# Optimization experiments

Hardware: AMD Instinct MI355X
Metric: run time of the kernel (lower is better)

## Reference

```python
import jax, jax.numpy as jnp
import numpy as np

N, A, H, W = 8, 3, 336, 336
IMG_W, IMG_H = 1333.0, 800.0
PRE_TOP_K = 2000
POST_NMS_TOP_N = 1000
NMS_THR = 0.7
MIN_SIZE = 0.0
TO_REMOVE = 1.0
XFORM_CLIP = float(np.log(1000.0 / 16.0))
NEG = -1e9


def setup_inputs() -> dict:
    key = jax.random.key(0)
    k1, k2, k3, k4, k5, k6 = jax.random.split(key, 6)
    M = A * H * W
    x1 = jax.random.uniform(k1, (N, M)) * (IMG_W - 1.0)
    y1 = jax.random.uniform(k2, (N, M)) * (IMG_H - 1.0)
    bw = jax.random.uniform(k3, (N, M)) * 256.0 + 4.0
    bh = jax.random.uniform(k4, (N, M)) * 256.0 + 4.0
    anchors = jnp.stack([x1, y1, x1 + bw, y1 + bh], axis=-1).astype(jnp.float32)
    logits = jax.random.normal(k5, (N, A, H, W), dtype=jnp.float32)
    bbox_reg = jax.random.normal(k6, (N, A * 4, H, W), dtype=jnp.float32) * 0.25
    return {"anchors": anchors, "logits": logits, "bbox_reg": bbox_reg}


def _decode(anchors, deltas):
    # anchors, deltas: [..., 4] in xyxy / (dx,dy,dw,dh)
    w = anchors[..., 2] - anchors[..., 0] + TO_REMOVE
    h = anchors[..., 3] - anchors[..., 1] + TO_REMOVE
    cx = anchors[..., 0] + 0.5 * w
    cy = anchors[..., 1] + 0.5 * h
    dx, dy, dw, dh = deltas[..., 0], deltas[..., 1], deltas[..., 2], deltas[..., 3]
    dw = jnp.minimum(dw, XFORM_CLIP)
    dh = jnp.minimum(dh, XFORM_CLIP)
    pcx = dx * w + cx
    pcy = dy * h + cy
    pw = jnp.exp(dw) * w
    ph = jnp.exp(dh) * h
    return jnp.stack([pcx - 0.5 * pw, pcy - 0.5 * ph,
                      pcx + 0.5 * pw - 1.0, pcy + 0.5 * ph - 1.0], axis=-1)


def _nms_single(boxes, scores):
    # boxes: [K,4], scores: [K] (invalid entries already set to NEG)
    areas = (boxes[:, 2] - boxes[:, 0] + TO_REMOVE) * (boxes[:, 3] - boxes[:, 1] + TO_REMOVE)

    def step(live, _):
        j = jnp.argmax(live)
        sj = live[j]
        bj = boxes[j]
        xx1 = jnp.maximum(bj[0], boxes[:, 0])
        yy1 = jnp.maximum(bj[1], boxes[:, 1])
        xx2 = jnp.minimum(bj[2], boxes[:, 2])
        yy2 = jnp.minimum(bj[3], boxes[:, 3])
        inter = jnp.maximum(xx2 - xx1 + TO_REMOVE, 0.0) * jnp.maximum(yy2 - yy1 + TO_REMOVE, 0.0)
        iou = inter / (areas[j] + areas - inter)
        live = jnp.where(iou > NMS_THR, NEG, live)
        live = live.at[j].set(NEG)
        valid = sj > NEG * 0.5
        return live, (jnp.where(valid, bj, 0.0), jnp.where(valid, sj, 0.0))

    _, (sel_boxes, sel_scores) = jax.lax.scan(step, scores, None, length=POST_NMS_TOP_N)
    return sel_boxes, sel_scores


def _forward(anchors, logits, bbox_reg):
    n, a, h, w = logits.shape
    # objectness scores: [N, A*H*W], ordered as (H, W, A) like the torch permute
    scores = jax.nn.sigmoid(jnp.transpose(logits, (0, 2, 3, 1)).reshape(n, -1))
    reg = bbox_reg.reshape(n, a, 4, h, w)
    reg = jnp.transpose(reg, (0, 3, 4, 1, 2)).reshape(n, -1, 4)
    k = min(scores.shape[1], PRE_TOP_K)
    top_scores, idx = jax.lax.top_k(scores, k)  # sorted descending
    reg_k = jnp.take_along_axis(reg, idx[..., None], axis=1)
    anc_k = jnp.take_along_axis(anchors, idx[..., None], axis=1)
    props = _decode(anc_k, reg_k)
    x1 = jnp.clip(props[..., 0], 0.0, IMG_W - 1.0)
    y1 = jnp.clip(props[..., 1], 0.0, IMG_H - 1.0)
    x2 = jnp.clip(props[..., 2], 0.0, IMG_W - 1.0)
    y2 = jnp.clip(props[..., 3], 0.0, IMG_H - 1.0)
    clipped = jnp.stack([x1, y1, x2, y2], axis=-1)
    ws = x2 - x1 + TO_REMOVE
    hs = y2 - y1 + TO_REMOVE
    keep = (ws >= MIN_SIZE) & (hs >= MIN_SIZE)
    sc = jnp.where(keep, top_scores, NEG)
    sel_boxes, sel_scores = jax.vmap(_nms_single)(clipped, sc)
    # [N, POST_NMS_TOP_N, 5] = boxes + score
    return jnp.concatenate([sel_boxes, sel_scores[..., None]], axis=-1)


def reference(anchors, logits, bbox_reg):
    return _forward(anchors, logits, bbox_reg)
```

## Files before the change

### kernel.cpp

```cpp
#include <hip/hip_runtime.h>
#include <stdint.h>

#define N_BATCH 8
#define A_ 3
#define H_ 336
#define W_ 336
#define HW_ (H_*W_)
#define M_ (A_*HW_)
#define K_TOP 2000
#define POST_N 1000
#define NMS_THR_ 0.7f
#define NEG_ (-1e9f)
#define VALID_THR_ (-5e8f)
#define CAND_CAP 4096
#define NBINS 4096
#define BIN_SHIFT 20
#define HBLK 32
#define SEG_ (M_/HBLK)
#define XCLIP 4.135166556742356f

#define NPAD 2048
#define NW 32
#define NCHUNK 32
#define RING 4
#define RBLK 128

typedef unsigned long long u64;

__device__ __forceinline__ unsigned int flip_key(float x) {
    unsigned int u = __float_as_uint(x);
    return (u & 0x80000000u) ? ~u : (u | 0x80000000u);
}
__device__ __forceinline__ float unflip_key(unsigned int k) {
    unsigned int u = (k & 0x80000000u) ? (k & 0x7fffffffu) : ~k;
    return __uint_as_float(u);
}

__device__ __forceinline__ void gload_lds16(const u64* g, u64* l) {
    __builtin_amdgcn_global_load_lds(
        (const __attribute__((address_space(1))) unsigned int*)(const void*)g,
        (__attribute__((address_space(3))) unsigned int*)(void*)l,
        16, 0, 0);
}

__global__ __launch_bounds__(512) void k_hist(const float* __restrict__ logits,
                                              unsigned short* __restrict__ ghist,
                                              unsigned int* __restrict__ cnt) {
    __shared__ unsigned int h[NBINS];
    int n = blockIdx.y, b = blockIdx.x;
    if (b == 0 && threadIdx.x == 0) cnt[n] = 0;
    for (int i = threadIdx.x; i < NBINS; i += 512) h[i] = 0;
    __syncthreads();
    const float4* lp = (const float4*)(logits + (size_t)n * M_ + (size_t)b * SEG_);
    const int nq = SEG_ / 4;
    for (int q = threadIdx.x; q < nq; q += 512) {
        float4 v = lp[q];
        atomicAdd(&h[flip_key(v.x) >> BIN_SHIFT], 1u);
        atomicAdd(&h[flip_key(v.y) >> BIN_SHIFT], 1u);
        atomicAdd(&h[flip_key(v.z) >> BIN_SHIFT], 1u);
        atomicAdd(&h[flip_key(v.w) >> BIN_SHIFT], 1u);
    }
    __syncthreads();
    unsigned short* gp = ghist + ((size_t)n * HBLK + b) * NBINS;
    for (int i = threadIdx.x; i < NBINS; i += 512) gp[i] = (unsigned short)h[i];
}

__global__ __launch_bounds__(512) void k_compact(const float* __restrict__ logits,
                                                 const unsigned short* __restrict__ ghist,
                                                 unsigned int* __restrict__ cnt,
                                                 u64* __restrict__ cand) {
    __shared__ unsigned int binsum[NBINS];
    __shared__ unsigned int part[512];
    __shared__ unsigned int scanb[512];
    __shared__ u64 buf[CAND_CAP];
    __shared__ unsigned int lcnt;
    __shared__ unsigned int gbase;
    __shared__ int Bsh;
    int n = blockIdx.y, b = blockIdx.x;
    int t = threadIdx.x;
    if (t == 0) lcnt = 0;
    const unsigned short* base = ghist + (size_t)n * HBLK * NBINS;
    for (int i = t; i < NBINS; i += 512) {
        unsigned int s = 0;
        #pragma unroll 8
        for (int sb = 0; sb < HBLK; ++sb) s += base[(size_t)sb * NBINS + i];
        binsum[i] = s;
    }
    __syncthreads();
    int hi = NBINS - 8 * t;
    int lo = hi - 8;
    unsigned int s = 0;
    for (int bb = lo; bb < hi; ++bb) s += binsum[bb];
    part[t] = s;
    scanb[t] = s;
    __syncthreads();
    for (int off = 1; off < 512; off <<= 1) {
        unsigned int v = scanb[t];
        unsigned int addv = (t >= off) ? scanb[t - off] : 0u;
        __syncthreads();
        scanb[t] = v + addv;
        __syncthreads();
    }
    unsigned int incl = scanb[t];
    unsigned int prefix = incl - part[t];
    if (prefix < K_TOP && incl >= K_TOP) {
        unsigned int acc = prefix;
        for (int bb = hi - 1; bb >= lo; --bb) {
            unsigned int c = binsum[bb];
            if (acc + c >= K_TOP) { Bsh = bb; break; }
            acc += c;
        }
    }
    __syncthreads();
    unsigned int B = (unsigned int)Bsh;
    const int qbase = b * SEG_;
    const float4* lp = (const float4*)(logits + (size_t)n * M_ + (size_t)qbase);
    const int nq = SEG_ / 4;
    for (int q = t; q < nq; q += 512) {
        float4 v = lp[q];
        float vv[4] = {v.x, v.y, v.z, v.w};
        #pragma unroll
        for (int e = 0; e < 4; ++e) {
            unsigned int u = flip_key(vv[e]);
            if ((u >> BIN_SHIFT) >= B) {
                int qq = qbase + q * 4 + e;
                int a = qq / HW_;
                int hw = qq - a * HW_;
                unsigned int m = (unsigned int)(hw * A_ + a);
                unsigned int pos = atomicAdd(&lcnt, 1u);
                if (pos < CAND_CAP)
                    buf[pos] = ((u64)u << 32) | (unsigned int)(~m);
            }
        }
    }
    __syncthreads();
    unsigned int L = (lcnt < CAND_CAP) ? lcnt : CAND_CAP;
    if (t == 0) gbase = atomicAdd(&cnt[n], L);
    __syncthreads();
    u64* cp = cand + (size_t)n * CAND_CAP;
    for (unsigned int i = t; i < L; i += 512) {
        unsigned int pos = gbase + i;
        if (pos < CAND_CAP) cp[pos] = buf[i];
    }
}

__global__ __launch_bounds__(512) void k_rank(const u64* __restrict__ cand,
                                              const unsigned int* __restrict__ cnt,
                                              const float* __restrict__ anchors,
                                              const float* __restrict__ breg,
                                              float4* __restrict__ boxes,
                                              float* __restrict__ scores,
                                              float* __restrict__ areas) {
    __shared__ u64 keys[CAND_CAP];
    __shared__ unsigned short psum[512];
    int n = blockIdx.y;
    int bx = blockIdx.x;
    unsigned int Cu = cnt[n];
    int C = (Cu < CAND_CAP) ? (int)Cu : CAND_CAP;
    if (bx * RBLK >= C) return;
    const u64* cp = cand + (size_t)n * CAND_CAP;
    for (int i = threadIdx.x; i < C; i += 512) keys[i] = cp[i];
    __syncthreads();
    int t = threadIdx.x;
    int tq = t & 3;
    int cl = t >> 2;
    int ci = bx * RBLK + cl;
    unsigned int r = 0;
    u64 ki = 0;
    if (ci < C) {
        ki = keys[ci];
        int j = tq;
        for (; j + 12 < C; j += 16) {
            r += (keys[j] > ki);
            r += (keys[j + 4] > ki);
            r += (keys[j + 8] > ki);
            r += (keys[j + 12] > ki);
        }
        for (; j < C; j += 4) r += (keys[j] > ki);
    }
    psum[t] = (unsigned short)r;
    __syncthreads();
    if (tq == 0 && ci < C) {
        unsigned int rank = (unsigned int)psum[t] + psum[t + 1] + psum[t + 2] + psum[t + 3];
        if (rank < K_TOP) {
            unsigned int u = (unsigned int)(ki >> 32);
            unsigned int m = ~((unsigned int)ki);
            float logit = unflip_key(u);
            int a = (int)(m % 3u);
            int hw = (int)(m / 3u);
            float4 anc = ((const float4*)anchors)[(size_t)n * M_ + m];
            size_t rb = ((size_t)n * 12 + a * 4) * HW_ + hw;
            float dx = breg[rb];
            float dy = breg[rb + (size_t)HW_];
            float dw = breg[rb + (size_t)2 * HW_];
            float dh = breg[rb + (size_t)3 * HW_];
            float score = 1.0f / (1.0f + expf(-logit));
            float w = anc.z - anc.x + 1.0f;
            float h = anc.w - anc.y + 1.0f;
            float cx = anc.x + 0.5f * w;
            float cy = anc.y + 0.5f * h;
            dw = fminf(dw, XCLIP);
            dh = fminf(dh, XCLIP);
            float pcx = dx * w + cx;
            float pcy = dy * h + cy;
            float pw = expf(dw) * w;
            float ph = expf(dh) * h;
            float x1 = pcx - 0.5f * pw;
            float y1 = pcy - 0.5f * ph;
            float x2 = pcx + 0.5f * pw - 1.0f;
            float y2 = pcy + 0.5f * ph - 1.0f;
            x1 = fminf(fmaxf(x1, 0.0f), 1332.0f);
            y1 = fminf(fmaxf(y1, 0.0f), 799.0f);
            x2 = fminf(fmaxf(x2, 0.0f), 1332.0f);
            y2 = fminf(fmaxf(y2, 0.0f), 799.0f);
            float ww = x2 - x1 + 1.0f;
            float hh = y2 - y1 + 1.0f;
            bool keep = (ww >= 0.0f) && (hh >= 0.0f);
            int g = n * K_TOP + (int)rank;
            boxes[g] = make_float4(x1, y1, x2, y2);
            scores[g] = keep ? score : NEG_;
            areas[g] = ww * hh;
        }
    }
}

#define JT 512
#define RT 64
__global__ __launch_bounds__(256) void k_edges(const float4* __restrict__ boxes,
                                               const float* __restrict__ areas,
                                               u64* __restrict__ adj) {
    int n = blockIdx.z;
    int by = blockIdx.y;
    int bx = blockIdx.x;
    if (by > bx * 8 + 7) return;
    __shared__ float4 jb[JT];
    __shared__ float ja[JT];
    int r0 = by * RT;
    int j0 = bx * JT;
    for (int j = threadIdx.x; j < JT; j += 256) {
        int jj = j0 + j;
        if (jj < K_TOP) {
            jb[j] = boxes[(size_t)n * K_TOP + jj];
            ja[j] = areas[(size_t)n * K_TOP + jj];
        } else {
            jb[j] = make_float4(-1e8f, -1e8f, -1e8f, -1e8f);
            ja[j] = 0.0f;
        }
    }
    __syncthreads();
    int i = r0 + (threadIdx.x >> 2);
    if (i >= K_TOP) return;
    float4 bi = boxes[(size_t)n * K_TOP + i];
    float ai = areas[(size_t)n * K_TOP + i];
    #pragma unroll
    for (int rep = 0; rep < 2; ++rep) {
        int wl = (threadIdx.x & 3) + rep * 4;
        u64 bits = 0;
        int base = wl * 64;
        #pragma unroll 8
        for (int b = 0; b < 64; ++b) {
            float4 bj = jb[base + b];
            float xx1 = fmaxf(bi.x, bj.x);
            float yy1 = fmaxf(bi.y, bj.y);
            float xx2 = fminf(bi.z, bj.z);
            float yy2 = fminf(bi.w, bj.w);
            float inter = fmaxf(xx2 - xx1 + 1.0f, 0.0f) * fmaxf(yy2 - yy1 + 1.0f, 0.0f);
            float iou = inter / (ai + ja[base + b] - inter);
            bits |= ((u64)(iou > NMS_THR_)) << b;
        }
        adj[((size_t)n * NPAD + i) * NW + (j0 >> 6) + wl] = bits;
    }
}

__global__ __launch_bounds__(256) void k_resolve(const float4* __restrict__ boxes,
                                                 const float* __restrict__ scores,
                                                 const u64* __restrict__ adj,
                                                 float* __restrict__ out) {
    __shared__ u64 ring[RING][64 * NW];
    __shared__ float sls[NPAD];
    __shared__ unsigned char alive[NPAD];
    __shared__ int ready[RING];
    __shared__ int progress;
    __shared__ unsigned int scanbuf[256];
    int n = blockIdx.x;
    int tid = threadIdx.x;
    int wave = tid >> 6, lane = tid & 63;
    const u64* ab = adj + (size_t)n * NPAD * NW;

    for (int i = tid; i < NPAD; i += 256) {
        sls[i] = (i < K_TOP) ? scores[(size_t)n * K_TOP + i] : NEG_;
        alive[i] = 0;
    }
    if (tid < RING) ready[tid] = 0;
    if (tid == 0) progress = 0;
    __syncthreads();

    if (wave == 0) {
        u64 supreg = 0;
        int survTot = 0;
        for (int c = 0; c < NCHUNK; ++c) {
            int slot = c & (RING - 1);
            while (__hip_atomic_load(&ready[slot], __ATOMIC_ACQUIRE,
                                     __HIP_MEMORY_SCOPE_WORKGROUP) != c + 1)
                __builtin_amdgcn_s_sleep(1);
            int k = lane;
            int gi = c * 64 + k;
            u64 colk = ring[slot][k * NW + c];
            u64 supc = __shfl(supreg, c, 64);
            bool validk = (sls[gi] > VALID_THR_) && !((supc >> k) & 1ull);
            u64 below = (k == 0) ? 0ull : ((1ull << k) - 1ull);
            u64 rel = colk & below;
            bool a = validk;
            u64 am = __ballot(a);
            while (true) {
                bool anew = validk && ((am & rel) == 0ull);
                u64 am2 = __ballot(anew);
                if (am2 == am) { a = anew; break; }
                am = am2;
            }
            alive[gi] = a ? 1 : 0;
            int nal = (int)__popcll(am);
            survTot += nal;
            if (survTot >= POST_N) {
                if (lane == 0)
                    __hip_atomic_store(&progress, NCHUNK, __ATOMIC_RELEASE,
                                       __HIP_MEMORY_SCOPE_WORKGROUP);
                break;
            }
            int w = lane & 31, half = lane >> 5;
            u64 acc = 0;
            u64 m = am & (half ? 0xAAAAAAAAAAAAAAAAull : 0x5555555555555555ull);
            while (m) {
                int k1 = __ffsll((unsigned long long)m) - 1; m &= m - 1;
                int k2 = k1, k3 = k1, k4 = k1;
                if (m) { k2 = __ffsll((unsigned long long)m) - 1; m &= m - 1; }
                if (m) { k3 = __ffsll((unsigned long long)m) - 1; m &= m - 1; }
                if (m) { k4 = __ffsll((unsigned long long)m) - 1; m &= m - 1; }
                u64 r1 = ring[slot][k1 * NW + w];
                u64 r2 = ring[slot][k2 * NW + w];
                u64 r3 = ring[slot][k3 * NW + w];
                u64 r4 = ring[slot][k4 * NW + w];
                acc |= r1 | r2 | r3 | r4;
            }
            acc |= __shfl_down(acc, 32);
            if (lane < 32) supreg |= acc;
            if (lane == 0)
                __hip_atomic_store(&progress, c + 1, __ATOMIC_RELEASE,
                                   __HIP_MEMORY_SCOPE_WORKGROUP);
        }
    } else {
        for (int c = wave - 1; c < NCHUNK; c += 3) {
            int slot = c & (RING - 1);
            int p;
            while ((p = __hip_atomic_load(&progress, __ATOMIC_ACQUIRE,
                                          __HIP_MEMORY_SCOPE_WORKGROUP)) < c - 3)
                __builtin_amdgcn_s_sleep(1);
            if (p >= NCHUNK) break;
            const u64* src = ab + (size_t)c * 64 * NW + lane * 2;
            u64* dst = &ring[slot][0];
            #pragma unroll
            for (int it = 0; it < 16; ++it)
                gload_lds16(src + (size_t)it * 128, dst + it * 128);
            __builtin_amdgcn_s_waitcnt(0);
            if (lane == 0)
                __hip_atomic_store(&ready[slot], c + 1, __ATOMIC_RELEASE,
                                   __HIP_MEMORY_SCOPE_WORKGROUP);
        }
    }
    __syncthreads();

    int i0 = tid * 8;
    unsigned int c2 = 0;
    for (int i = i0; i < i0 + 8; ++i) c2 += alive[i];
    scanbuf[tid] = c2;
    __syncthreads();
    for (int off = 1; off < 256; off <<= 1) {
        unsigned int v = scanbuf[tid];
        unsigned int addv = (tid >= off) ? scanbuf[tid - off] : 0u;
        __syncthreads();
        scanbuf[tid] = v + addv;
        __syncthreads();
    }
    unsigned int r = scanbuf[tid] - c2;
    unsigned int total = scanbuf[255];
    float* op = out + (size_t)n * POST_N * 5;
    const float4* bb = boxes + (size_t)n * K_TOP;
    for (int i = i0; i < i0 + 8; ++i) {
        if (alive[i]) {
            if (r < POST_N) {
                float4 b = bb[i];
                op[r * 5 + 0] = b.x;
                op[r * 5 + 1] = b.y;
                op[r * 5 + 2] = b.z;
                op[r * 5 + 3] = b.w;
                op[r * 5 + 4] = sls[i];
            }
            r++;
        }
    }
    unsigned int S = (total > POST_N) ? POST_N : total;
    for (unsigned int q = S + tid; q < POST_N; q += 256) {
        op[q * 5 + 0] = 0.0f;
        op[q * 5 + 1] = 0.0f;
        op[q * 5 + 2] = 0.0f;
        op[q * 5 + 3] = 0.0f;
        op[q * 5 + 4] = 0.0f;
    }
}

extern "C" void kernel_launch(void* const* d_in, const int* in_sizes, int n_in,
                              void* d_out, int out_size, void* d_ws, size_t ws_size,
                              hipStream_t stream) {
    const float* anchors = (const float*)d_in[0];
    const float* logits  = (const float*)d_in[1];
    const float* breg    = (const float*)d_in[2];
    float* out = (float*)d_out;
    char* ws = (char*)d_ws;

    unsigned int* cnt     = (unsigned int*)(ws);
    unsigned short* ghist = (unsigned short*)(ws + 128);
    u64* cand             = (u64*)(ws + 2097280);
    u64* adj              = (u64*)(ws + 128);
    float4* boxes         = (float4*)(ws + 4194432);
    float* scores         = (float*)(ws + 4450432);
    float* areas          = (float*)(ws + 4514432);

    k_hist<<<dim3(HBLK, 8), 512, 0, stream>>>(logits, ghist, cnt);
    k_compact<<<dim3(HBLK, 8), 512, 0, stream>>>(logits, ghist, cnt, cand);
    k_rank<<<dim3(CAND_CAP / RBLK, 8), 512, 0, stream>>>(cand, cnt, anchors, breg,
                                                         boxes, scores, areas);
    k_edges<<<dim3(NPAD / JT, NPAD / RT, 8), 256, 0, stream>>>(boxes, areas, adj);
    k_resolve<<<8, 256, 0, stream>>>(boxes, scores, adj, out);
}
```

Before: 197.7 us.

## Split candidates into above-threshold and boundary-bin sets; dual LDS histograms; unroll suppression gather

After: 195.7 us. Within noise of the previous version (-1.1%).

```diff
diff --git a/kernel.cpp b/kernel.cpp
--- a/kernel.cpp
+++ b/kernel.cpp
@@ -46,23 +46,26 @@
 __global__ __launch_bounds__(512) void k_hist(const float* __restrict__ logits,
                                               unsigned short* __restrict__ ghist,
                                               unsigned int* __restrict__ cnt) {
-    __shared__ unsigned int h[NBINS];
+    __shared__ unsigned int h[2][NBINS];
     int n = blockIdx.y, b = blockIdx.x;
-    if (b == 0 && threadIdx.x == 0) cnt[n] = 0;
-    for (int i = threadIdx.x; i < NBINS; i += 512) h[i] = 0;
-    __syncthreads();
+    if (b == 0 && threadIdx.x < 2) cnt[n * 2 + threadIdx.x] = 0;
+    unsigned int* hf = &h[0][0];
+    for (int i = threadIdx.x; i < 2 * NBINS; i += 512) hf[i] = 0;
+    __syncthreads();
+    int wp = (threadIdx.x >> 6) & 1;
     const float4* lp = (const float4*)(logits + (size_t)n * M_ + (size_t)b * SEG_);
     const int nq = SEG_ / 4;
     for (int q = threadIdx.x; q < nq; q += 512) {
         float4 v = lp[q];
-        atomicAdd(&h[flip_key(v.x) >> BIN_SHIFT], 1u);
-        atomicAdd(&h[flip_key(v.y) >> BIN_SHIFT], 1u);
-        atomicAdd(&h[flip_key(v.z) >> BIN_SHIFT], 1u);
-        atomicAdd(&h[flip_key(v.w) >> BIN_SHIFT], 1u);
+        atomicAdd(&h[wp][flip_key(v.x) >> BIN_SHIFT], 1u);
+        atomicAdd(&h[wp][flip_key(v.y) >> BIN_SHIFT], 1u);
+        atomicAdd(&h[wp][flip_key(v.z) >> BIN_SHIFT], 1u);
+        atomicAdd(&h[wp][flip_key(v.w) >> BIN_SHIFT], 1u);
     }
     __syncthreads();
     unsigned short* gp = ghist + ((size_t)n * HBLK + b) * NBINS;
-    for (int i = threadIdx.x; i < NBINS; i += 512) gp[i] = (unsigned short)h[i];
+    for (int i = threadIdx.x; i < NBINS; i += 512)
+        gp[i] = (unsigned short)(h[0][i] + h[1][i]);
 }
 
 __global__ __launch_bounds__(512) void k_compact(const float* __restrict__ logits,
@@ -72,13 +75,13 @@
     __shared__ unsigned int binsum[NBINS];
     __shared__ unsigned int part[512];
     __shared__ unsigned int scanb[512];
-    __shared__ u64 buf[CAND_CAP];
-    __shared__ unsigned int lcnt;
-    __shared__ unsigned int gbase;
+    __shared__ u64 bufHi[2048];
+    __shared__ u64 bufLo[4096];
+    __shared__ unsigned int lcntHi, lcntLo, gbaseHi, gbaseLo;
     __shared__ int Bsh;
     int n = blockIdx.y, b = blockIdx.x;
     int t = threadIdx.x;
-    if (t == 0) lcnt = 0;
+    if (t == 0) { lcntHi = 0; lcntLo = 0; }
     const unsigned short* base = ghist + (size_t)n * HBLK * NBINS;
     for (int i = t; i < NBINS; i += 512) {
         unsigned int s = 0;
@@ -122,25 +125,35 @@
         #pragma unroll
         for (int e = 0; e < 4; ++e) {
             unsigned int u = flip_key(vv[e]);
-            if ((u >> BIN_SHIFT) >= B) {
+            unsigned int bin = u >> BIN_SHIFT;
+            if (bin >= B) {
                 int qq = qbase + q * 4 + e;
                 int a = qq / HW_;
                 int hw = qq - a * HW_;
                 unsigned int m = (unsigned int)(hw * A_ + a);
-                unsigned int pos = atomicAdd(&lcnt, 1u);
-                if (pos < CAND_CAP)
-                    buf[pos] = ((u64)u << 32) | (unsigned int)(~m);
+                u64 key = ((u64)u << 32) | (unsigned int)(~m);
+                if (bin > B) {
+                    unsigned int pos = atomicAdd(&lcntHi, 1u);
+                    if (pos < 2048) bufHi[pos] = key;
+                } else {
+                    unsigned int pos = atomicAdd(&lcntLo, 1u);
+                    if (pos < 4096) bufLo[pos] = key;
+                }
             }
         }
     }
     __syncthreads();
-    unsigned int L = (lcnt < CAND_CAP) ? lcnt : CAND_CAP;
-    if (t == 0) gbase = atomicAdd(&cnt[n], L);
+    unsigned int Lhi = (lcntHi < 2048u) ? lcntHi : 2048u;
+    unsigned int Llo = (lcntLo < 4096u) ? lcntLo : 4096u;
+    if (t == 0) gbaseHi = atomicAdd(&cnt[n * 2], Lhi);
+    if (t == 1) gbaseLo = atomicAdd(&cnt[n * 2 + 1], Llo);
     __syncthreads();
     u64* cp = cand + (size_t)n * CAND_CAP;
-    for (unsigned int i = t; i < L; i += 512) {
-        unsigned int pos = gbase + i;
-        if (pos < CAND_CAP) cp[pos] = buf[i];
+    for (unsigned int i = t; i < Lhi; i += 512)
+        cp[gbaseHi + i] = bufHi[i];
+    for (unsigned int i = t; i < Llo; i += 512) {
+        unsigned int idx = CAND_CAP - 1u - (gbaseLo + i);
+        if ((int)idx >= K_TOP) cp[idx] = bufLo[i];
     }
 }
 
@@ -155,33 +168,40 @@
     __shared__ unsigned short psum[512];
     int n = blockIdx.y;
     int bx = blockIdx.x;
-    unsigned int Cu = cnt[n];
-    int C = (Cu < CAND_CAP) ? (int)Cu : CAND_CAP;
-    if (bx * RBLK >= C) return;
+    unsigned int T = cnt[n * 2];
+    unsigned int Lc = cnt[n * 2 + 1];
+    unsigned int Ls = (Lc < (unsigned int)(CAND_CAP - K_TOP)) ? Lc : (unsigned int)(CAND_CAP - K_TOP);
+    int loStart = CAND_CAP - (int)Ls;
+    int p0 = bx * RBLK;
+    if (p0 >= (int)T && p0 + RBLK <= loStart) return;
     const u64* cp = cand + (size_t)n * CAND_CAP;
-    for (int i = threadIdx.x; i < C; i += 512) keys[i] = cp[i];
+    for (int i = threadIdx.x; i < (int)T; i += 512) keys[i] = cp[i];
+    for (int i = loStart + threadIdx.x; i < CAND_CAP; i += 512) keys[i] = cp[i];
     __syncthreads();
     int t = threadIdx.x;
     int tq = t & 3;
     int cl = t >> 2;
-    int ci = bx * RBLK + cl;
+    int ci = p0 + cl;
+    bool isHi = (ci < (int)T);
+    bool isLo = (!isHi) && (ci >= loStart) && (ci < CAND_CAP);
     unsigned int r = 0;
     u64 ki = 0;
-    if (ci < C) {
-        ki = keys[ci];
-        int j = tq;
-        for (; j + 12 < C; j += 16) {
-            r += (keys[j] > ki);
-            r += (keys[j + 4] > ki);
-            r += (keys[j + 8] > ki);
-            r += (keys[j + 12] > ki);
-        }
-        for (; j < C; j += 4) r += (keys[j] > ki);
-    }
+    int jb = 0, je = 0;
+    unsigned int radd = 0;
+    if (isHi) { ki = keys[ci]; jb = 0; je = (int)T; }
+    else if (isLo) { ki = keys[ci]; jb = loStart; je = CAND_CAP; radd = T; }
+    int j = jb + tq;
+    for (; j + 12 < je; j += 16) {
+        r += (keys[j] > ki);
+        r += (keys[j + 4] > ki);
+        r += (keys[j + 8] > ki);
+        r += (keys[j + 12] > ki);
+    }
+    for (; j < je; j += 4) r += (keys[j] > ki);
     psum[t] = (unsigned short)r;
     __syncthreads();
-    if (tq == 0 && ci < C) {
-        unsigned int rank = (unsigned int)psum[t] + psum[t + 1] + psum[t + 2] + psum[t + 3];
+    if (tq == 0 && (isHi || isLo)) {
+        unsigned int rank = radd + psum[t] + psum[t + 1] + psum[t + 2] + psum[t + 3];
         if (rank < K_TOP) {
             unsigned int u = (unsigned int)(ki >> 32);
             unsigned int m = ~((unsigned int)ki);
@@ -331,16 +351,22 @@
             u64 acc = 0;
             u64 m = am & (half ? 0xAAAAAAAAAAAAAAAAull : 0x5555555555555555ull);
             while (m) {
-                int k1 = __ffsll((unsigned long long)m) - 1; m &= m - 1;
-                int k2 = k1, k3 = k1, k4 = k1;
-                if (m) { k2 = __ffsll((unsigned long long)m) - 1; m &= m - 1; }
-                if (m) { k3 = __ffsll((unsigned long long)m) - 1; m &= m - 1; }
-                if (m) { k4 = __ffsll((unsigned long long)m) - 1; m &= m - 1; }
-                u64 r1 = ring[slot][k1 * NW + w];
-                u64 r2 = ring[slot][k2 * NW + w];
-                u64 r3 = ring[slot][k3 * NW + w];
-                u64 r4 = ring[slot][k4 * NW + w];
-                acc |= r1 | r2 | r3 | r4;
+                int kk[8];
+                kk[0] = __ffsll((unsigned long long)m) - 1; m &= m - 1;
+                #pragma unroll
+                for (int e = 1; e < 8; ++e) {
+                    kk[e] = m ? (__ffsll((unsigned long long)m) - 1) : kk[0];
+                    if (m) m &= m - 1;
+                }
+                u64 r0 = ring[slot][kk[0] * NW + w];
+                u64 r1 = ring[slot][kk[1] * NW + w];
+                u64 r2 = ring[slot][kk[2] * NW + w];
+                u64 r3 = ring[slot][kk[3] * NW + w];
+                u64 r4 = ring[slot][kk[4] * NW + w];
+                u64 r5 = ring[slot][kk[5] * NW + w];
+                u64 r6 = ring[slot][kk[6] * NW + w];
+                u64 r7 = ring[slot][kk[7] * NW + w];
+                acc |= (r0 | r1) | (r2 | r3) | ((r4 | r5) | (r6 | r7));
             }
             acc |= __shfl_down(acc, 32);
             if (lane < 32) supreg |= acc;
```
